# Performance work log

Measured on AMD Instinct MI355X. Metric: run time of the kernel, lower is better.

The kernel has to match this reference:

```python
import jax, jax.numpy as jnp
import numpy as np

B, S, D = 16, 4096, 1024
K = 65536  # number of keys == number of concepts (identity mapping)
EPS = 1e-12


def setup_inputs() -> dict:
    key = jax.random.key(0)
    k1, k2, k3, k4, k5, k6 = jax.random.split(key, 6)
    return {
        "hidden": jax.random.normal(k1, (B, S, D), dtype=jnp.float32),
        "concept_signal": jax.random.normal(k2, (B, 1, D), dtype=jnp.float32),
        "keys": jax.random.normal(k3, (K, D), dtype=jnp.float32),
        "values": jax.random.normal(k4, (K, 1, D), dtype=jnp.float32),
        "key_to_value": jnp.arange(K, dtype=jnp.int64),
        "W_layer": jax.random.normal(k5, (D, D), dtype=jnp.float32) * 0.02,
        "b_layer": jax.random.normal(k6, (D,), dtype=jnp.float32) * 0.02,
    }


def _l2norm(x, axis=-1):
    return x / jnp.maximum(jnp.linalg.norm(x, axis=axis, keepdims=True), EPS)


def reference(hidden, concept_signal, keys, values, key_to_value, W_layer, b_layer):
    # self.layer(hidden_state): Linear(D, D)
    layer_out = jnp.einsum("bsd,ed->bse", hidden, W_layer) + b_layer  # [B, S, D]

    # Tensor branch of forward: per-sample nearest-key search.
    # q: one query position per sample (P=1) -> [B, D]
    q = concept_signal[:, 0, :]
    cos = jnp.einsum("bd,kd->bk", _l2norm(q), _l2norm(keys))  # cosine similarity [B, K]
    dist = 1.0 - cos                                           # cosine distance
    chosen_key = jnp.argmin(dist, axis=1)                      # [B] nearest key per sample
    # s = 1 - smallest_dist; with threshold=-2.0 it always passes; with
    # max_tokens_per_concept=1, k = max(1, ceil(clamp(s,0,1)*1)) == 1 token.
    concept_idx = key_to_value[chosen_key]                     # [B]
    tokens = values[concept_idx, 0, :]                         # [B, D] (first of the k=1 tokens)
    tokens = _l2norm(tokens)                                   # F.normalize(..., p=2, dim=-1)
    # vstack one token onto each sample, then stack -> [B, S+1, D]
    return jnp.concatenate([layer_out, tokens[:, None, :]], axis=1)
```

## Files before the change

kernel.cpp:

```cpp
#include <hip/hip_runtime.h>

constexpr int BB = 16;
constexpr int SS = 4096;
constexpr int DD = 1024;
constexpr int KK = 65536;
constexpr int GM = BB * SS;
constexpr int GK = DD;

typedef __attribute__((ext_vector_type(8))) short bf16x8;
typedef __attribute__((ext_vector_type(4))) float f32x4;
typedef __attribute__((ext_vector_type(8))) unsigned short ushort8;

#define GLD_LDS16(g, l)                                                        \
  __builtin_amdgcn_global_load_lds(                                            \
      (const __attribute__((address_space(1))) void*)(g),                      \
      (__attribute__((address_space(3))) void*)(l), 16, 0, 0)

__device__ __forceinline__ unsigned short f2bf(float x) {
  unsigned u = __float_as_uint(x);
  u += 0x7fffu + ((u >> 16) & 1u);
  return (unsigned short)(u >> 16);
}

__global__ void cvt_bf16(const float* __restrict__ in,
                         unsigned short* __restrict__ out, int n8) {
  int stride = gridDim.x * blockDim.x;
  for (int i = blockIdx.x * blockDim.x + threadIdx.x; i < n8; i += stride) {
    const float4* p = (const float4*)in + (size_t)i * 2;
    float4 a = p[0], b = p[1];
    ushort8 r;
    r[0] = f2bf(a.x); r[1] = f2bf(a.y); r[2] = f2bf(a.z); r[3] = f2bf(a.w);
    r[4] = f2bf(b.x); r[5] = f2bf(b.y); r[6] = f2bf(b.z); r[7] = f2bf(b.w);
    *(ushort8*)(out + (size_t)i * 8) = r;
  }
}

__global__ __launch_bounds__(256) void qt_prep(const float* __restrict__ csig,
                                               float* __restrict__ qT) {
  int e = blockIdx.x * 256 + threadIdx.x;
  int b = e >> 10, d = e & 1023;
  qT[d * 16 + b] = csig[e];
}


#define LDA8(AH, BUF) do {                                                     \
  _Pragma("unroll") for (int ms = 0; ms < 4; ++ms) {                           \
    int rowa = (wm << 7) + ((AH) << 6) + (ms << 4) + fr;                       \
    _Pragma("unroll") for (int ks = 0; ks < 2; ++ks) {                         \
      int ia = ((rowa << 6) + (ks << 5) + (kg << 3)) ^ sw;                     \
      ar[ms * 2 + ks] = *(const bf16x8*)&lds[(BUF) + ia]; } }                  \
} while (0)

#define LDB4(NP, BUF) do {                                                     \
  _Pragma("unroll") for (int nn = 0; nn < 2; ++nn) {                           \
    int rowb = (wn << 6) + ((((NP) << 1) + nn) << 4) + fr;                     \
    _Pragma("unroll") for (int ks = 0; ks < 2; ++ks) {                         \
      int ib = ((rowb << 6) + (ks << 5) + (kg << 3)) ^ sw;                     \
      br[(((NP) << 1) + nn) * 2 + ks] = *(const bf16x8*)&lds[(BUF) + ib]; } }  \
} while (0)

#define MFMAQ(AH, NP) do {                                                     \
  _Pragma("unroll") for (int ms = 0; ms < 4; ++ms)                             \
  _Pragma("unroll") for (int nn = 0; nn < 2; ++nn)                             \
  _Pragma("unroll") for (int ks = 0; ks < 2; ++ks)                             \
    acc[((AH) << 2) + ms][((NP) << 1) + nn] =                                  \
      __builtin_amdgcn_mfma_f32_16x16x32_bf16(ar[ms * 2 + ks],                 \
        br[(((NP) << 1) + nn) * 2 + ks],                                       \
        acc[((AH) << 2) + ms][((NP) << 1) + nn], 0, 0, 0);                     \
} while (0)

#define STAGEQ(GB, LB, QJ)                                                     \
  GLD_LDS16((GB) + (size_t)(((QJ) << 6) + srq) * GK + ssc,                     \
            &lds[(LB) + ((((QJ) << 9) + (wv << 6)) << 3)])

#define PH_MID do { __builtin_amdgcn_s_barrier();                              \
  asm volatile("s_waitcnt lgkmcnt(0)" ::: "memory");                           \
  __builtin_amdgcn_sched_barrier(0);                                           \
  __builtin_amdgcn_s_setprio(1); } while (0)

#define PH_END do { __builtin_amdgcn_s_setprio(0);                             \
  __builtin_amdgcn_s_barrier(); } while (0)

#define PH_END_V(N) do { __builtin_amdgcn_s_setprio(0);                        \
  asm volatile("s_waitcnt vmcnt(" #N ")" ::: "memory");                        \
  __builtin_amdgcn_sched_barrier(0);                                           \
  __builtin_amdgcn_s_barrier(); } while (0)

__global__ __launch_bounds__(512, 2) void gemm8(
    const unsigned short* __restrict__ A,
    const unsigned short* __restrict__ Bm,
    const float* __restrict__ bias,
    float* __restrict__ out) {
  __shared__ unsigned short lds[65536];

  int g = blockIdx.x;
  int t = ((g & 7) << 7) + (g >> 3);
  int mt = t >> 2, nt = t & 3;
  int m0 = mt << 8, n0 = nt << 8;

  int tid = threadIdx.x, lane = tid & 63, wv = tid >> 6;
  int wm = wv >> 2, wn = wv & 3;
  int fr = lane & 15, kg = lane >> 4;
  int sw = (fr & 7) << 3;

  int srq = (wv << 3) + (lane >> 3);
  int ssc = (((lane & 7) ^ ((lane >> 3) & 7)) << 3);

  const unsigned short* Ag = A + (size_t)m0 * GK;
  const unsigned short* Bg = Bm + (size_t)n0 * GK;

  f32x4 acc[8][4] = {};
  bf16x8 ar[8], br[8];

  {
    const unsigned short* b0 = Bg;
    const unsigned short* a1 = Ag + 64;
    const unsigned short* b1 = Bg + 64;
    STAGEQ(Ag, 0, 0); STAGEQ(Ag, 0, 1); STAGEQ(Ag, 0, 2); STAGEQ(Ag, 0, 3);
    STAGEQ(b0, 16384, 0); STAGEQ(b0, 16384, 1);
    STAGEQ(b0, 16384, 2); STAGEQ(b0, 16384, 3);
    STAGEQ(a1, 32768, 0); STAGEQ(a1, 32768, 2);
    STAGEQ(b1, 49152, 0); STAGEQ(b1, 49152, 1);
    STAGEQ(b1, 49152, 2); STAGEQ(b1, 49152, 3);
    asm volatile("s_waitcnt vmcnt(6)" ::: "memory");
    __builtin_amdgcn_sched_barrier(0);
    __builtin_amdgcn_s_barrier();
  }

  for (int i = 0; i < 7; ++i) {
    const unsigned short* a1 = Ag + (size_t)(2 * i + 1) * 64;
    const unsigned short* a2 = Ag + (size_t)(2 * i + 2) * 64;
    const unsigned short* b2 = Bg + (size_t)(2 * i + 2) * 64;
    const unsigned short* a3 = Ag + (size_t)(2 * i + 3) * 64;
    const unsigned short* b3 = Bg + (size_t)(2 * i + 3) * 64;
    LDA8(0, 0); LDB4(0, 16384);
    STAGEQ(a1, 32768, 1); STAGEQ(a1, 32768, 3);
    PH_MID; MFMAQ(0, 0); PH_END;
    LDB4(1, 16384);
    STAGEQ(a2, 0, 0); STAGEQ(a2, 0, 2);
    PH_MID; MFMAQ(0, 1); PH_END;
    LDA8(1, 0);
    STAGEQ(b2, 16384, 0); STAGEQ(b2, 16384, 1);
    PH_MID; MFMAQ(1, 0); PH_END;
    STAGEQ(b2, 16384, 2); STAGEQ(b2, 16384, 3);
    PH_MID; MFMAQ(1, 1); PH_END_V(6);
    LDA8(0, 32768); LDB4(0, 49152);
    STAGEQ(a2, 0, 1); STAGEQ(a2, 0, 3);
    PH_MID; MFMAQ(0, 0); PH_END;
    LDB4(1, 49152);
    STAGEQ(a3, 32768, 0); STAGEQ(a3, 32768, 2);
    PH_MID; MFMAQ(0, 1); PH_END;
    LDA8(1, 32768);
    STAGEQ(b3, 49152, 0); STAGEQ(b3, 49152, 1);
    PH_MID; MFMAQ(1, 0); PH_END;
    STAGEQ(b3, 49152, 2); STAGEQ(b3, 49152, 3);
    PH_MID; MFMAQ(1, 1); PH_END_V(6);
  }

  {
    const unsigned short* a15 = Ag + (size_t)15 * 64;
    LDA8(0, 0); LDB4(0, 16384);
    STAGEQ(a15, 32768, 1); STAGEQ(a15, 32768, 3);
    PH_MID; MFMAQ(0, 0); PH_END;
    LDB4(1, 16384); PH_MID; MFMAQ(0, 1); PH_END;
    LDA8(1, 0);     PH_MID; MFMAQ(1, 0); PH_END;
    PH_MID; MFMAQ(1, 1); PH_END_V(0);
    LDA8(0, 32768); LDB4(0, 49152); PH_MID; MFMAQ(0, 0); PH_END;
    LDB4(1, 49152); PH_MID; MFMAQ(0, 1); PH_END;
    LDA8(1, 32768); PH_MID; MFMAQ(1, 0); PH_END;
    PH_MID; MFMAQ(1, 1);
    __builtin_amdgcn_s_setprio(0);
  }

  int r0 = kg << 2, cc = fr;
#pragma unroll
  for (int ni = 0; ni < 4; ++ni) {
    int gcol = n0 + (wn << 6) + (ni << 4) + cc;
    float bv = bias[gcol];
#pragma unroll
    for (int mi = 0; mi < 8; ++mi) {
      int gr = m0 + (wm << 7) + (mi << 4) + r0;
#pragma unroll
      for (int j = 0; j < 4; ++j) {
        int grow = gr + j;
        size_t o = ((size_t)(grow + (grow >> 12)) << 10) + gcol;
        out[o] = acc[mi][ni][j] + bv;
      }
    }
  }
}

__global__ __launch_bounds__(256) void cos_part4(
    const float* __restrict__ keys,
    const float* __restrict__ qT,
    float* __restrict__ pd,
    float* __restrict__ pn) {
  __shared__ float kt[32][256];
  __shared__ float qs[256 * 16];

  int tid = threadIdx.x;
  int kgrp = blockIdx.x & 255, dc = blockIdx.x >> 8;
  int k0 = kgrp << 8, d0 = dc << 8;

  {
    const float4* src = (const float4*)(qT + (size_t)d0 * 16);
    float4* dst = (float4*)qs;
#pragma unroll
    for (int i = 0; i < 4; ++i) dst[tid + i * 256] = src[tid + i * 256];
  }

  float acc[16] = {0.f, 0.f, 0.f, 0.f, 0.f, 0.f, 0.f, 0.f,
                   0.f, 0.f, 0.f, 0.f, 0.f, 0.f, 0.f, 0.f};
  float nrm = 0.f;

  int srow = tid >> 3, scol = (tid & 7) << 2;
  const float* gsrc = keys + (size_t)(k0 + srow) * DD + d0 + scol;

  float4 stg[8];
#pragma unroll
  for (int i = 0; i < 8; ++i)
    stg[i] = *(const float4*)(gsrc + (size_t)i * 32 * DD);

  for (int t = 0; t < 8; ++t) {
#pragma unroll
    for (int i = 0; i < 8; ++i) {
      int r = (i << 5) + srow;
#pragma unroll
      for (int j = 0; j < 4; ++j) {
        int dd = scol + j;
        kt[dd][r ^ (((dd >> 2) & 7) << 2)] = stg[i][j];
      }
    }
    __syncthreads();

    if (t + 1 < 8) {
#pragma unroll
      for (int i = 0; i < 8; ++i)
        stg[i] = *(const float4*)(gsrc + (size_t)i * 32 * DD + (t + 1) * 32);
    }

    const float* qb = qs + (t << 5) * 16;
#pragma unroll
    for (int dd = 0; dd < 32; ++dd) {
      float kv = kt[dd][tid ^ (((dd >> 2) & 7) << 2)];
      float4 q0 = *(const float4*)(qb + dd * 16 + 0);
      float4 q1 = *(const float4*)(qb + dd * 16 + 4);
      float4 q2 = *(const float4*)(qb + dd * 16 + 8);
      float4 q3 = *(const float4*)(qb + dd * 16 + 12);
      acc[0]  = fmaf(kv, q0.x, acc[0]);  acc[1]  = fmaf(kv, q0.y, acc[1]);
      acc[2]  = fmaf(kv, q0.z, acc[2]);  acc[3]  = fmaf(kv, q0.w, acc[3]);
      acc[4]  = fmaf(kv, q1.x, acc[4]);  acc[5]  = fmaf(kv, q1.y, acc[5]);
      acc[6]  = fmaf(kv, q1.z, acc[6]);  acc[7]  = fmaf(kv, q1.w, acc[7]);
      acc[8]  = fmaf(kv, q2.x, acc[8]);  acc[9]  = fmaf(kv, q2.y, acc[9]);
      acc[10] = fmaf(kv, q2.z, acc[10]); acc[11] = fmaf(kv, q2.w, acc[11]);
      acc[12] = fmaf(kv, q3.x, acc[12]); acc[13] = fmaf(kv, q3.y, acc[13]);
      acc[14] = fmaf(kv, q3.z, acc[14]); acc[15] = fmaf(kv, q3.w, acc[15]);
      nrm = fmaf(kv, kv, nrm);
    }
    __syncthreads();
  }

  int k = k0 + tid;
  float4* po = (float4*)(pd + ((size_t)dc * KK + k) * 16);
  po[0] = make_float4(acc[0], acc[1], acc[2], acc[3]);
  po[1] = make_float4(acc[4], acc[5], acc[6], acc[7]);
  po[2] = make_float4(acc[8], acc[9], acc[10], acc[11]);
  po[3] = make_float4(acc[12], acc[13], acc[14], acc[15]);
  pn[(size_t)dc * KK + k] = nrm;
}

__global__ __launch_bounds__(256) void cos_combine(
    const float* __restrict__ pd, const float* __restrict__ pn,
    float* __restrict__ pscore, int* __restrict__ pidx) {
  __shared__ float rs[4][16];
  __shared__ int ri[4][16];
  int tid = threadIdx.x, lane = tid & 63, w = tid >> 6;
  int k = blockIdx.x * 256 + tid;

  float d[16] = {0.f, 0.f, 0.f, 0.f, 0.f, 0.f, 0.f, 0.f,
                 0.f, 0.f, 0.f, 0.f, 0.f, 0.f, 0.f, 0.f};
  float nrm = 0.f;
#pragma unroll
  for (int dc = 0; dc < 4; ++dc) {
    const float4* p = (const float4*)(pd + ((size_t)dc * KK + k) * 16);
#pragma unroll
    for (int i = 0; i < 4; ++i) {
      float4 v = p[i];
      d[i * 4 + 0] += v.x; d[i * 4 + 1] += v.y;
      d[i * 4 + 2] += v.z; d[i * 4 + 3] += v.w;
    }
    nrm += pn[(size_t)dc * KK + k];
  }
  float inv = rsqrtf(fmaxf(nrm, 1e-24f));

#pragma unroll
  for (int b = 0; b < 16; ++b) {
    float s = d[b] * inv;
    int i = k;
#pragma unroll
    for (int off = 32; off; off >>= 1) {
      float s2 = __shfl_xor(s, off);
      int i2 = __shfl_xor(i, off);
      if (s2 > s || (s2 == s && i2 < i)) { s = s2; i = i2; }
    }
    if (lane == 0) { rs[w][b] = s; ri[w][b] = i; }
  }
  __syncthreads();
  if (tid < 16) {
    float bs = rs[0][tid]; int bi = ri[0][tid];
#pragma unroll
    for (int w2 = 1; w2 < 4; ++w2) {
      float s = rs[w2][tid]; int i = ri[w2][tid];
      if (s > bs || (s == bs && i < bi)) { bs = s; bi = i; }
    }
    pscore[(size_t)tid * gridDim.x + blockIdx.x] = bs;
    pidx[(size_t)tid * gridDim.x + blockIdx.x] = bi;
  }
}

__global__ __launch_bounds__(256) void select_write(
    const float* __restrict__ pscore, const int* __restrict__ pidx, int nb,
    const int* __restrict__ ktv, const float* __restrict__ values,
    float* __restrict__ out) {
  __shared__ float ss[4];
  __shared__ int si[4];
  __shared__ float snrm;
  __shared__ int swin;
  int b = blockIdx.x, tid = threadIdx.x, lane = tid & 63, wv = tid >> 6;

  float best = -1e30f;
  int bidx = 0x7fffffff;
  for (int t = tid; t < nb; t += 256) {
    float s = pscore[(size_t)b * nb + t];
    int i = pidx[(size_t)b * nb + t];
    if (s > best || (s == best && i < bidx)) { best = s; bidx = i; }
  }
#pragma unroll
  for (int off = 32; off; off >>= 1) {
    float s = __shfl_xor(best, off);
    int i = __shfl_xor(bidx, off);
    if (s > best || (s == best && i < bidx)) { best = s; bidx = i; }
  }
  if (lane == 0) { ss[wv] = best; si[wv] = bidx; }
  __syncthreads();
  if (tid == 0) {
    float bs = ss[0]; int bi = si[0];
    for (int w2 = 1; w2 < 4; ++w2)
      if (ss[w2] > bs || (ss[w2] == bs && si[w2] < bi)) { bs = ss[w2]; bi = si[w2]; }
    swin = ktv[bi];
  }
  __syncthreads();
  int idx = swin;

  float4 v = ((const float4*)(values + (size_t)idx * DD))[tid];
  float nrm = v.x * v.x + v.y * v.y + v.z * v.z + v.w * v.w;
#pragma unroll
  for (int off = 32; off; off >>= 1) nrm += __shfl_xor(nrm, off);
  if (lane == 0) ss[wv] = nrm;
  __syncthreads();
  if (tid == 0) snrm = rsqrtf(fmaxf(ss[0] + ss[1] + ss[2] + ss[3], 1e-24f));
  __syncthreads();
  float inv = snrm;

  float4 o;
  o.x = v.x * inv; o.y = v.y * inv; o.z = v.z * inv; o.w = v.w * inv;
  ((float4*)(out + (((size_t)b * (SS + 1) + SS) << 10)))[tid] = o;
}

extern "C" void kernel_launch(void* const* d_in, const int* in_sizes, int n_in,
                              void* d_out, int out_size, void* d_ws,
                              size_t ws_size, hipStream_t stream) {
  const float* hidden = (const float*)d_in[0];
  const float* csig   = (const float*)d_in[1];
  const float* keys   = (const float*)d_in[2];
  const float* values = (const float*)d_in[3];
  const int*   ktv    = (const int*)d_in[4];
  const float* W      = (const float*)d_in[5];
  const float* bias   = (const float*)d_in[6];
  float* out = (float*)d_out;

  char* ws = (char*)d_ws;
  size_t off = 0;
  unsigned short* hbf = (unsigned short*)(ws + off); off += (size_t)GM * GK * 2;
  unsigned short* wbf = (unsigned short*)(ws + off); off += (size_t)DD * GK * 2;
  float* pd     = (float*)(ws + off); off += (size_t)4 * KK * 16 * 4;
  float* pn     = (float*)(ws + off); off += (size_t)4 * KK * 4;
  float* pscore = (float*)(ws + off); off += (size_t)16 * 256 * 4;
  int*   pidx   = (int*)(ws + off);   off += (size_t)16 * 256 * 4;
  float* qT     = (float*)(ws + off); off += (size_t)DD * 16 * 4;

  cvt_bf16<<<4096, 256, 0, stream>>>(hidden, hbf, GM * GK / 8);
  cvt_bf16<<<512, 256, 0, stream>>>(W, wbf, DD * GK / 8);
  qt_prep<<<64, 256, 0, stream>>>(csig, qT);

  cos_part4<<<1024, 256, 0, stream>>>(keys, qT, pd, pn);
  cos_combine<<<256, 256, 0, stream>>>(pd, pn, pscore, pidx);

  gemm8<<<1024, 512, 0, stream>>>(hbf, wbf, bias, out);

  select_write<<<BB, 256, 0, stream>>>(pscore, pidx, 256, ktv, values, out);
}
```

Measured before the change: 396.5 us.

## Fuse fp32-to-bf16 conversion of hidden into GEMM A-tile staging

Drops the separate pass that converts the large hidden tensor to bf16. The GEMM now loads fp32 A tiles into registers, converts them in-kernel and writes bf16 to LDS, software-pipelined against the MFMA phases. This removes a full read and write of a 256 MB-scale intermediate and one launch. In exchange the GEMM reads twice the bytes for A, uses more VGPRs for the staging registers, and replaces async global-to-LDS loads with register round trips, which could hurt occupancy or overlap.

After: 573.4 us. +44.6%, slower.

```diff
diff --git a/kernel.cpp b/kernel.cpp
--- a/kernel.cpp
+++ b/kernel.cpp
@@ -73,12 +73,32 @@
   GLD_LDS16((GB) + (size_t)(((QJ) << 6) + srq) * GK + ssc,                     \
             &lds[(LB) + ((((QJ) << 9) + (wv << 6)) << 3)])
 
+#define ALD(R, TP, QA, QB) do {                                                \
+  const float* pa_ = (TP) + (size_t)(((QA) << 6) + srq) * GK + ssc;            \
+  const float* pb_ = (TP) + (size_t)(((QB) << 6) + srq) * GK + ssc;            \
+  R[0] = *(const float4*)pa_; R[1] = *(const float4*)(pa_ + 4);                \
+  R[2] = *(const float4*)pb_; R[3] = *(const float4*)(pb_ + 4);                \
+} while (0)
+
+#define AWR(LB, QA, QB, R) do {                                                \
+  ushort8 w0_, w1_;                                                            \
+  w0_[0] = f2bf(R[0].x); w0_[1] = f2bf(R[0].y); w0_[2] = f2bf(R[0].z);         \
+  w0_[3] = f2bf(R[0].w); w0_[4] = f2bf(R[1].x); w0_[5] = f2bf(R[1].y);         \
+  w0_[6] = f2bf(R[1].z); w0_[7] = f2bf(R[1].w);                                \
+  w1_[0] = f2bf(R[2].x); w1_[1] = f2bf(R[2].y); w1_[2] = f2bf(R[2].z);         \
+  w1_[3] = f2bf(R[2].w); w1_[4] = f2bf(R[3].x); w1_[5] = f2bf(R[3].y);         \
+  w1_[6] = f2bf(R[3].z); w1_[7] = f2bf(R[3].w);                                \
+  *(ushort8*)&lds[(LB) + ((((QA) << 9) + (wv << 6)) << 3) + (lane << 3)] = w0_;\
+  *(ushort8*)&lds[(LB) + ((((QB) << 9) + (wv << 6)) << 3) + (lane << 3)] = w1_;\
+} while (0)
+
 #define PH_MID do { __builtin_amdgcn_s_barrier();                              \
   asm volatile("s_waitcnt lgkmcnt(0)" ::: "memory");                           \
   __builtin_amdgcn_sched_barrier(0);                                           \
   __builtin_amdgcn_s_setprio(1); } while (0)
 
 #define PH_END do { __builtin_amdgcn_s_setprio(0);                             \
+  __builtin_amdgcn_sched_barrier(0);                                           \
   __builtin_amdgcn_s_barrier(); } while (0)
 
 #define PH_END_V(N) do { __builtin_amdgcn_s_setprio(0);                        \
@@ -87,7 +107,7 @@
   __builtin_amdgcn_s_barrier(); } while (0)
 
 __global__ __launch_bounds__(512, 2) void gemm8(
-    const unsigned short* __restrict__ A,
+    const float* __restrict__ A,
     const unsigned short* __restrict__ Bm,
     const float* __restrict__ bias,
     float* __restrict__ out) {
@@ -106,70 +126,64 @@
   int srq = (wv << 3) + (lane >> 3);
   int ssc = (((lane & 7) ^ ((lane >> 3) & 7)) << 3);
 
-  const unsigned short* Ag = A + (size_t)m0 * GK;
+  const float* Ag = A + (size_t)m0 * GK;
   const unsigned short* Bg = Bm + (size_t)n0 * GK;
 
   f32x4 acc[8][4] = {};
   bf16x8 ar[8], br[8];
+  float4 sAX[4], sAY[4];
 
   {
-    const unsigned short* b0 = Bg;
-    const unsigned short* a1 = Ag + 64;
-    const unsigned short* b1 = Bg + 64;
-    STAGEQ(Ag, 0, 0); STAGEQ(Ag, 0, 1); STAGEQ(Ag, 0, 2); STAGEQ(Ag, 0, 3);
-    STAGEQ(b0, 16384, 0); STAGEQ(b0, 16384, 1);
-    STAGEQ(b0, 16384, 2); STAGEQ(b0, 16384, 3);
-    STAGEQ(a1, 32768, 0); STAGEQ(a1, 32768, 2);
-    STAGEQ(b1, 49152, 0); STAGEQ(b1, 49152, 1);
-    STAGEQ(b1, 49152, 2); STAGEQ(b1, 49152, 3);
-    asm volatile("s_waitcnt vmcnt(6)" ::: "memory");
-    __builtin_amdgcn_sched_barrier(0);
-    __builtin_amdgcn_s_barrier();
-  }
-
-  for (int i = 0; i < 7; ++i) {
-    const unsigned short* a1 = Ag + (size_t)(2 * i + 1) * 64;
-    const unsigned short* a2 = Ag + (size_t)(2 * i + 2) * 64;
-    const unsigned short* b2 = Bg + (size_t)(2 * i + 2) * 64;
-    const unsigned short* a3 = Ag + (size_t)(2 * i + 3) * 64;
-    const unsigned short* b3 = Bg + (size_t)(2 * i + 3) * 64;
+    const float* a1 = Ag + 64;
+    const float* a2 = Ag + 128;
+    STAGEQ(Bg, 16384, 0); STAGEQ(Bg, 16384, 1);
+    STAGEQ(Bg, 16384, 2); STAGEQ(Bg, 16384, 3);
+    STAGEQ(Bg + 64, 49152, 0); STAGEQ(Bg + 64, 49152, 1);
+    STAGEQ(Bg + 64, 49152, 2); STAGEQ(Bg + 64, 49152, 3);
+    ALD(sAX, Ag, 0, 2); ALD(sAY, Ag, 1, 3);
+    AWR(0, 0, 2, sAX);  AWR(0, 1, 3, sAY);
+    ALD(sAX, a1, 0, 2);
+    AWR(32768, 0, 2, sAX);
+    ALD(sAX, a1, 1, 3);
+    ALD(sAY, a2, 0, 2);
+    __syncthreads();
+  }
+
+  for (int i = 0; i < 8; ++i) {
+    int e2 = 2 * i + 2 > 15 ? 15 : 2 * i + 2;
+    int o2 = 2 * i + 3 > 15 ? 15 : 2 * i + 3;
+    int e4 = 2 * i + 4 > 15 ? 15 : 2 * i + 4;
+    const float* aE2 = Ag + (size_t)e2 * 64;
+    const float* aO2 = Ag + (size_t)o2 * 64;
+    const float* aE4 = Ag + (size_t)e4 * 64;
+    const unsigned short* bE2 = Bg + (size_t)e2 * 64;
+    const unsigned short* bO2 = Bg + (size_t)o2 * 64;
     LDA8(0, 0); LDB4(0, 16384);
-    STAGEQ(a1, 32768, 1); STAGEQ(a1, 32768, 3);
+    AWR(32768, 1, 3, sAX);
     PH_MID; MFMAQ(0, 0); PH_END;
     LDB4(1, 16384);
-    STAGEQ(a2, 0, 0); STAGEQ(a2, 0, 2);
+    AWR(0, 0, 2, sAY);
     PH_MID; MFMAQ(0, 1); PH_END;
     LDA8(1, 0);
-    STAGEQ(b2, 16384, 0); STAGEQ(b2, 16384, 1);
+    ALD(sAX, aE2, 1, 3);
+    STAGEQ(bE2, 16384, 0); STAGEQ(bE2, 16384, 1);
     PH_MID; MFMAQ(1, 0); PH_END;
-    STAGEQ(b2, 16384, 2); STAGEQ(b2, 16384, 3);
-    PH_MID; MFMAQ(1, 1); PH_END_V(6);
+    ALD(sAY, aO2, 0, 2);
+    STAGEQ(bE2, 16384, 2); STAGEQ(bE2, 16384, 3);
+    PH_MID; MFMAQ(1, 1); PH_END_V(12);
     LDA8(0, 32768); LDB4(0, 49152);
-    STAGEQ(a2, 0, 1); STAGEQ(a2, 0, 3);
+    AWR(0, 1, 3, sAX);
     PH_MID; MFMAQ(0, 0); PH_END;
     LDB4(1, 49152);
-    STAGEQ(a3, 32768, 0); STAGEQ(a3, 32768, 2);
+    AWR(32768, 0, 2, sAY);
     PH_MID; MFMAQ(0, 1); PH_END;
     LDA8(1, 32768);
-    STAGEQ(b3, 49152, 0); STAGEQ(b3, 49152, 1);
+    ALD(sAX, aO2, 1, 3);
+    STAGEQ(bO2, 49152, 0); STAGEQ(bO2, 49152, 1);
     PH_MID; MFMAQ(1, 0); PH_END;
-    STAGEQ(b3, 49152, 2); STAGEQ(b3, 49152, 3);
-    PH_MID; MFMAQ(1, 1); PH_END_V(6);
-  }
-
-  {
-    const unsigned short* a15 = Ag + (size_t)15 * 64;
-    LDA8(0, 0); LDB4(0, 16384);
-    STAGEQ(a15, 32768, 1); STAGEQ(a15, 32768, 3);
-    PH_MID; MFMAQ(0, 0); PH_END;
-    LDB4(1, 16384); PH_MID; MFMAQ(0, 1); PH_END;
-    LDA8(1, 0);     PH_MID; MFMAQ(1, 0); PH_END;
-    PH_MID; MFMAQ(1, 1); PH_END_V(0);
-    LDA8(0, 32768); LDB4(0, 49152); PH_MID; MFMAQ(0, 0); PH_END;
-    LDB4(1, 49152); PH_MID; MFMAQ(0, 1); PH_END;
-    LDA8(1, 32768); PH_MID; MFMAQ(1, 0); PH_END;
-    PH_MID; MFMAQ(1, 1);
-    __builtin_amdgcn_s_setprio(0);
+    ALD(sAY, aE4, 0, 2);
+    STAGEQ(bO2, 49152, 2); STAGEQ(bO2, 49152, 3);
+    PH_MID; MFMAQ(1, 1); PH_END_V(12);
   }
 
   int r0 = kg << 2, cc = fr;
@@ -381,7 +395,6 @@
 
   char* ws = (char*)d_ws;
   size_t off = 0;
-  unsigned short* hbf = (unsigned short*)(ws + off); off += (size_t)GM * GK * 2;
   unsigned short* wbf = (unsigned short*)(ws + off); off += (size_t)DD * GK * 2;
   float* pd     = (float*)(ws + off); off += (size_t)4 * KK * 16 * 4;
   float* pn     = (float*)(ws + off); off += (size_t)4 * KK * 4;
@@ -389,14 +402,13 @@
   int*   pidx   = (int*)(ws + off);   off += (size_t)16 * 256 * 4;
   float* qT     = (float*)(ws + off); off += (size_t)DD * 16 * 4;
 
-  cvt_bf16<<<4096, 256, 0, stream>>>(hidden, hbf, GM * GK / 8);
   cvt_bf16<<<512, 256, 0, stream>>>(W, wbf, DD * GK / 8);
   qt_prep<<<64, 256, 0, stream>>>(csig, qT);
 
   cos_part4<<<1024, 256, 0, stream>>>(keys, qT, pd, pn);
   cos_combine<<<256, 256, 0, stream>>>(pd, pn, pscore, pidx);
 
-  gemm8<<<1024, 512, 0, stream>>>(hbf, wbf, bias, out);
+  gemm8<<<1024, 512, 0, stream>>>(hidden, wbf, bias, out);
 
   select_write<<<BB, 256, 0, stream>>>(pscore, pidx, 256, ktv, values, out);
 }
```

## Fuse cosine partials and bf16 conversions into one heterogeneous prep launch

Applied to the files above, without the earlier changes.

Merges the key-similarity partial kernel and the hidden and W bf16 conversions into a single launch. Block ranges pick which job a block runs, so the memory-bound conversion overlaps the similarity work and two launches go away. The query transpose kernel is removed, and the cosine loop now reads concept_signal straight from global memory with broadcast loads instead of staging it in LDS. A fallback path reuses workspace when it is too small. The risk is slower query reads and load imbalance between the two kinds of block.

After: 412.1 us. 3.9% more time.

```diff
diff --git a/kernel.cpp b/kernel.cpp
--- a/kernel.cpp
+++ b/kernel.cpp
@@ -22,24 +22,107 @@
   return (unsigned short)(u >> 16);
 }
 
+__device__ __forceinline__ void cvt_body(const float* __restrict__ in,
+                                         unsigned short* __restrict__ out,
+                                         int i) {
+  const float4* p = (const float4*)in + (size_t)i * 2;
+  float4 a = p[0], b = p[1];
+  ushort8 r;
+  r[0] = f2bf(a.x); r[1] = f2bf(a.y); r[2] = f2bf(a.z); r[3] = f2bf(a.w);
+  r[4] = f2bf(b.x); r[5] = f2bf(b.y); r[6] = f2bf(b.z); r[7] = f2bf(b.w);
+  *(ushort8*)(out + (size_t)i * 8) = r;
+}
+
+__device__ __forceinline__ void cos_body(const float* __restrict__ keys,
+                                         const float* __restrict__ csig,
+                                         float* __restrict__ pd,
+                                         float* __restrict__ pn,
+                                         float (*kt)[256], int bid, int tid) {
+  int kgrp = bid & 255, dc = bid >> 8;
+  int k0 = kgrp << 8, d0 = dc << 8;
+
+  float acc[16] = {0.f, 0.f, 0.f, 0.f, 0.f, 0.f, 0.f, 0.f,
+                   0.f, 0.f, 0.f, 0.f, 0.f, 0.f, 0.f, 0.f};
+  float nrm = 0.f;
+
+  int srow = tid >> 3, scol = (tid & 7) << 2;
+  const float* gsrc = keys + (size_t)(k0 + srow) * DD + d0 + scol;
+
+  float4 stg[8];
+#pragma unroll
+  for (int i = 0; i < 8; ++i)
+    stg[i] = *(const float4*)(gsrc + (size_t)i * 32 * DD);
+
+  for (int t = 0; t < 8; ++t) {
+#pragma unroll
+    for (int i = 0; i < 8; ++i) {
+      int r = (i << 5) + srow;
+#pragma unroll
+      for (int j = 0; j < 4; ++j) {
+        int dd = scol + j;
+        kt[dd][r ^ (((dd >> 2) & 7) << 2)] = stg[i][j];
+      }
+    }
+    __syncthreads();
+
+    if (t + 1 < 8) {
+#pragma unroll
+      for (int i = 0; i < 8; ++i)
+        stg[i] = *(const float4*)(gsrc + (size_t)i * 32 * DD + (t + 1) * 32);
+    }
+
+    const float* qb = csig + d0 + (t << 5);
+#pragma unroll
+    for (int dd = 0; dd < 32; ++dd) {
+      float kv = kt[dd][tid ^ (((dd >> 2) & 7) << 2)];
+#pragma unroll
+      for (int b = 0; b < 16; ++b)
+        acc[b] = fmaf(kv, qb[(size_t)b * DD + dd], acc[b]);
+      nrm = fmaf(kv, kv, nrm);
+    }
+    __syncthreads();
+  }
+
+  int k = k0 + tid;
+  float4* po = (float4*)(pd + ((size_t)dc * KK + k) * 16);
+  po[0] = make_float4(acc[0], acc[1], acc[2], acc[3]);
+  po[1] = make_float4(acc[4], acc[5], acc[6], acc[7]);
+  po[2] = make_float4(acc[8], acc[9], acc[10], acc[11]);
+  po[3] = make_float4(acc[12], acc[13], acc[14], acc[15]);
+  pn[(size_t)dc * KK + k] = nrm;
+}
+
+__global__ __launch_bounds__(256) void prep_fused(
+    const float* __restrict__ keys, const float* __restrict__ csig,
+    float* __restrict__ pd, float* __restrict__ pn,
+    const float* __restrict__ hidden, unsigned short* __restrict__ hbf,
+    const float* __restrict__ W, unsigned short* __restrict__ wbf) {
+  __shared__ float kt[32][256];
+  int bid = blockIdx.x, tid = threadIdx.x;
+  if (bid < 1024) {
+    cos_body(keys, csig, pd, pn, kt, bid, tid);
+  } else if (bid < 5120) {
+    int base = (bid - 1024) * 256 + tid;
+#pragma unroll
+    for (int r = 0; r < 8; ++r)
+      cvt_body(hidden, hbf, base + r * (4096 * 256));
+  } else {
+    cvt_body(W, wbf, (bid - 5120) * 256 + tid);
+  }
+}
+
+__global__ __launch_bounds__(256) void cos_part4_k(
+    const float* __restrict__ keys, const float* __restrict__ csig,
+    float* __restrict__ pd, float* __restrict__ pn) {
+  __shared__ float kt[32][256];
+  cos_body(keys, csig, pd, pn, kt, blockIdx.x, threadIdx.x);
+}
+
 __global__ void cvt_bf16(const float* __restrict__ in,
                          unsigned short* __restrict__ out, int n8) {
   int stride = gridDim.x * blockDim.x;
-  for (int i = blockIdx.x * blockDim.x + threadIdx.x; i < n8; i += stride) {
-    const float4* p = (const float4*)in + (size_t)i * 2;
-    float4 a = p[0], b = p[1];
-    ushort8 r;
-    r[0] = f2bf(a.x); r[1] = f2bf(a.y); r[2] = f2bf(a.z); r[3] = f2bf(a.w);
-    r[4] = f2bf(b.x); r[5] = f2bf(b.y); r[6] = f2bf(b.z); r[7] = f2bf(b.w);
-    *(ushort8*)(out + (size_t)i * 8) = r;
-  }
-}
-
-__global__ __launch_bounds__(256) void qt_prep(const float* __restrict__ csig,
-                                               float* __restrict__ qT) {
-  int e = blockIdx.x * 256 + threadIdx.x;
-  int b = e >> 10, d = e & 1023;
-  qT[d * 16 + b] = csig[e];
+  for (int i = blockIdx.x * blockDim.x + threadIdx.x; i < n8; i += stride)
+    cvt_body(in, out, i);
 }
 
 
@@ -190,85 +273,6 @@
   }
 }
 
-__global__ __launch_bounds__(256) void cos_part4(
-    const float* __restrict__ keys,
-    const float* __restrict__ qT,
-    float* __restrict__ pd,
-    float* __restrict__ pn) {
-  __shared__ float kt[32][256];
-  __shared__ float qs[256 * 16];
-
-  int tid = threadIdx.x;
-  int kgrp = blockIdx.x & 255, dc = blockIdx.x >> 8;
-  int k0 = kgrp << 8, d0 = dc << 8;
-
-  {
-    const float4* src = (const float4*)(qT + (size_t)d0 * 16);
-    float4* dst = (float4*)qs;
-#pragma unroll
-    for (int i = 0; i < 4; ++i) dst[tid + i * 256] = src[tid + i * 256];
-  }
-
-  float acc[16] = {0.f, 0.f, 0.f, 0.f, 0.f, 0.f, 0.f, 0.f,
-                   0.f, 0.f, 0.f, 0.f, 0.f, 0.f, 0.f, 0.f};
-  float nrm = 0.f;
-
-  int srow = tid >> 3, scol = (tid & 7) << 2;
-  const float* gsrc = keys + (size_t)(k0 + srow) * DD + d0 + scol;
-
-  float4 stg[8];
-#pragma unroll
-  for (int i = 0; i < 8; ++i)
-    stg[i] = *(const float4*)(gsrc + (size_t)i * 32 * DD);
-
-  for (int t = 0; t < 8; ++t) {
-#pragma unroll
-    for (int i = 0; i < 8; ++i) {
-      int r = (i << 5) + srow;
-#pragma unroll
-      for (int j = 0; j < 4; ++j) {
-        int dd = scol + j;
-        kt[dd][r ^ (((dd >> 2) & 7) << 2)] = stg[i][j];
-      }
-    }
-    __syncthreads();
-
-    if (t + 1 < 8) {
-#pragma unroll
-      for (int i = 0; i < 8; ++i)
-        stg[i] = *(const float4*)(gsrc + (size_t)i * 32 * DD + (t + 1) * 32);
-    }
-
-    const float* qb = qs + (t << 5) * 16;
-#pragma unroll
-    for (int dd = 0; dd < 32; ++dd) {
-      float kv = kt[dd][tid ^ (((dd >> 2) & 7) << 2)];
-      float4 q0 = *(const float4*)(qb + dd * 16 + 0);
-      float4 q1 = *(const float4*)(qb + dd * 16 + 4);
-      float4 q2 = *(const float4*)(qb + dd * 16 + 8);
-      float4 q3 = *(const float4*)(qb + dd * 16 + 12);
-      acc[0]  = fmaf(kv, q0.x, acc[0]);  acc[1]  = fmaf(kv, q0.y, acc[1]);
-      acc[2]  = fmaf(kv, q0.z, acc[2]);  acc[3]  = fmaf(kv, q0.w, acc[3]);
-      acc[4]  = fmaf(kv, q1.x, acc[4]);  acc[5]  = fmaf(kv, q1.y, acc[5]);
-      acc[6]  = fmaf(kv, q1.z, acc[6]);  acc[7]  = fmaf(kv, q1.w, acc[7]);
-      acc[8]  = fmaf(kv, q2.x, acc[8]);  acc[9]  = fmaf(kv, q2.y, acc[9]);
-      acc[10] = fmaf(kv, q2.z, acc[10]); acc[11] = fmaf(kv, q2.w, acc[11]);
-      acc[12] = fmaf(kv, q3.x, acc[12]); acc[13] = fmaf(kv, q3.y, acc[13]);
-      acc[14] = fmaf(kv, q3.z, acc[14]); acc[15] = fmaf(kv, q3.w, acc[15]);
-      nrm = fmaf(kv, kv, nrm);
-    }
-    __syncthreads();
-  }
-
-  int k = k0 + tid;
-  float4* po = (float4*)(pd + ((size_t)dc * KK + k) * 16);
-  po[0] = make_float4(acc[0], acc[1], acc[2], acc[3]);
-  po[1] = make_float4(acc[4], acc[5], acc[6], acc[7]);
-  po[2] = make_float4(acc[8], acc[9], acc[10], acc[11]);
-  po[3] = make_float4(acc[12], acc[13], acc[14], acc[15]);
-  pn[(size_t)dc * KK + k] = nrm;
-}
-
 __global__ __launch_bounds__(256) void cos_combine(
     const float* __restrict__ pd, const float* __restrict__ pn,
     float* __restrict__ pscore, int* __restrict__ pidx) {
@@ -380,23 +384,37 @@
   float* out = (float*)d_out;
 
   char* ws = (char*)d_ws;
-  size_t off = 0;
-  unsigned short* hbf = (unsigned short*)(ws + off); off += (size_t)GM * GK * 2;
-  unsigned short* wbf = (unsigned short*)(ws + off); off += (size_t)DD * GK * 2;
-  float* pd     = (float*)(ws + off); off += (size_t)4 * KK * 16 * 4;
-  float* pn     = (float*)(ws + off); off += (size_t)4 * KK * 4;
-  float* pscore = (float*)(ws + off); off += (size_t)16 * 256 * 4;
-  int*   pidx   = (int*)(ws + off);   off += (size_t)16 * 256 * 4;
-  float* qT     = (float*)(ws + off); off += (size_t)DD * 16 * 4;
-
-  cvt_bf16<<<4096, 256, 0, stream>>>(hidden, hbf, GM * GK / 8);
-  cvt_bf16<<<512, 256, 0, stream>>>(W, wbf, DD * GK / 8);
-  qt_prep<<<64, 256, 0, stream>>>(csig, qT);
-
-  cos_part4<<<1024, 256, 0, stream>>>(keys, qT, pd, pn);
-  cos_combine<<<256, 256, 0, stream>>>(pd, pn, pscore, pidx);
-
-  gemm8<<<1024, 512, 0, stream>>>(hbf, wbf, bias, out);
-
-  select_write<<<BB, 256, 0, stream>>>(pscore, pidx, 256, ktv, values, out);
-}
+  const size_t HB = (size_t)GM * GK * 2;
+  const size_t WB = (size_t)DD * GK * 2;
+  const size_t PDB = (size_t)4 * KK * 16 * 4;
+  const size_t PNB = (size_t)4 * KK * 4;
+  const size_t PSB = (size_t)16 * 256 * 4;
+
+  unsigned short* hbf = (unsigned short*)ws;
+  unsigned short* wbf = (unsigned short*)(ws + HB);
+
+  if (ws_size >= HB + WB + PDB + PNB + 2 * PSB) {
+    float* pd     = (float*)(ws + HB + WB);
+    float* pn     = (float*)(ws + HB + WB + PDB);
+    float* pscore = (float*)(ws + HB + WB + PDB + PNB);
+    int*   pidx   = (int*)(ws + HB + WB + PDB + PNB + PSB);
+
+    prep_fused<<<5632, 256, 0, stream>>>(keys, csig, pd, pn,
+                                         hidden, hbf, W, wbf);
+    cos_combine<<<256, 256, 0, stream>>>(pd, pn, pscore, pidx);
+    gemm8<<<1024, 512, 0, stream>>>(hbf, wbf, bias, out);
+    select_write<<<BB, 256, 0, stream>>>(pscore, pidx, 256, ktv, values, out);
+  } else {
+    float* pd     = (float*)ws;
+    float* pn     = (float*)(ws + PDB);
+    float* pscore = (float*)(ws + HB + WB);
+    int*   pidx   = (int*)(ws + HB + WB + PSB);
+
+    cos_part4_k<<<1024, 256, 0, stream>>>(keys, csig, pd, pn);
+    cos_combine<<<256, 256, 0, stream>>>(pd, pn, pscore, pidx);
+    cvt_bf16<<<4096, 256, 0, stream>>>(hidden, hbf, GM * GK / 8);
+    cvt_bf16<<<512, 256, 0, stream>>>(W, wbf, DD * GK / 8);
+    gemm8<<<1024, 512, 0, stream>>>(hbf, wbf, bias, out);
+    select_write<<<BB, 256, 0, stream>>>(pscore, pidx, 256, ktv, values, out);
+  }
+}
```

## Compute cosine search with split-bf16 MFMA and fused per-block argmax

Applied to the files above, without the earlier changes.

Replaces the FP32 FMA cosine-similarity kernel and its separate combine pass with a single MFMA kernel. The kernel splits queries and keys into bf16 high and low parts and uses three bf16 MFMAs to approximate fp32 accuracy. It also computes key norms and a per-block argmax inline, which removes the partial-dot workspace round trip and one kernel launch. The risk is a small precision loss from the three-term split, which could change argmin ties, and more select_write partials to reduce (1024 instead of 256).

Measured after the change: 379.9 us. 1.04x faster.

```diff
diff --git a/kernel.cpp b/kernel.cpp
--- a/kernel.cpp
+++ b/kernel.cpp
@@ -22,24 +22,112 @@
   return (unsigned short)(u >> 16);
 }
 
+__device__ __forceinline__ void cvt_body(const float* __restrict__ in,
+                                         unsigned short* __restrict__ out,
+                                         int i) {
+  const float4* p = (const float4*)in + (size_t)i * 2;
+  float4 a = p[0], b = p[1];
+  ushort8 r;
+  r[0] = f2bf(a.x); r[1] = f2bf(a.y); r[2] = f2bf(a.z); r[3] = f2bf(a.w);
+  r[4] = f2bf(b.x); r[5] = f2bf(b.y); r[6] = f2bf(b.z); r[7] = f2bf(b.w);
+  *(ushort8*)(out + (size_t)i * 8) = r;
+}
+
 __global__ void cvt_bf16(const float* __restrict__ in,
                          unsigned short* __restrict__ out, int n8) {
   int stride = gridDim.x * blockDim.x;
-  for (int i = blockIdx.x * blockDim.x + threadIdx.x; i < n8; i += stride) {
-    const float4* p = (const float4*)in + (size_t)i * 2;
-    float4 a = p[0], b = p[1];
-    ushort8 r;
-    r[0] = f2bf(a.x); r[1] = f2bf(a.y); r[2] = f2bf(a.z); r[3] = f2bf(a.w);
-    r[4] = f2bf(b.x); r[5] = f2bf(b.y); r[6] = f2bf(b.z); r[7] = f2bf(b.w);
-    *(ushort8*)(out + (size_t)i * 8) = r;
-  }
-}
-
-__global__ __launch_bounds__(256) void qt_prep(const float* __restrict__ csig,
-                                               float* __restrict__ qT) {
-  int e = blockIdx.x * 256 + threadIdx.x;
-  int b = e >> 10, d = e & 1023;
-  qT[d * 16 + b] = csig[e];
+  for (int i = blockIdx.x * blockDim.x + threadIdx.x; i < n8; i += stride)
+    cvt_body(in, out, i);
+}
+
+__global__ __launch_bounds__(256) void qsplit(const float* __restrict__ csig,
+                                              unsigned short* __restrict__ qh,
+                                              unsigned short* __restrict__ ql) {
+  int i = blockIdx.x * 256 + threadIdx.x;
+  float v = csig[i];
+  unsigned short h = f2bf(v);
+  float hf = __uint_as_float((unsigned)h << 16);
+  qh[i] = h;
+  ql[i] = f2bf(v - hf);
+}
+
+__global__ __launch_bounds__(256) void cos_mfma(
+    const float* __restrict__ keys,
+    const unsigned short* __restrict__ qh,
+    const unsigned short* __restrict__ ql,
+    float* __restrict__ pscore,
+    int* __restrict__ pidx) {
+  __shared__ float rs[4][16];
+  __shared__ int ri[4][16];
+  int tid = threadIdx.x, lane = tid & 63, w = tid >> 6;
+  int fr = lane & 15, kg = lane >> 4;
+  int key = blockIdx.x * 64 + w * 16 + fr;
+
+  const float* krow = keys + (size_t)key * DD + kg * 8;
+  const unsigned short* qhp = qh + fr * DD + kg * 8;
+  const unsigned short* qlp = ql + fr * DD + kg * 8;
+
+  f32x4 acc = {};
+  float nrm = 0.f;
+
+  float4 ka = *(const float4*)krow;
+  float4 kb = *(const float4*)(krow + 4);
+  bf16x8 h8 = *(const bf16x8*)qhp;
+  bf16x8 l8 = *(const bf16x8*)qlp;
+
+  for (int t = 0; t < 32; ++t) {
+    float4 kc = ka, kd = kb;
+    bf16x8 hh = h8, ll = l8;
+    if (t + 1 < 32) {
+      ka = *(const float4*)(krow + (t + 1) * 32);
+      kb = *(const float4*)(krow + (t + 1) * 32 + 4);
+      h8 = *(const bf16x8*)(qhp + (t + 1) * 32);
+      l8 = *(const bf16x8*)(qlp + (t + 1) * 32);
+    }
+    float ke[8] = {kc.x, kc.y, kc.z, kc.w, kd.x, kd.y, kd.z, kd.w};
+    ushort8 khv, klv;
+#pragma unroll
+    for (int j = 0; j < 8; ++j) {
+      float v = ke[j];
+      unsigned short h = f2bf(v);
+      float hf = __uint_as_float((unsigned)h << 16);
+      khv[j] = h;
+      klv[j] = f2bf(v - hf);
+      nrm = fmaf(v, v, nrm);
+    }
+    bf16x8 kh8 = *(bf16x8*)&khv, kl8 = *(bf16x8*)&klv;
+    acc = __builtin_amdgcn_mfma_f32_16x16x32_bf16(hh, kh8, acc, 0, 0, 0);
+    acc = __builtin_amdgcn_mfma_f32_16x16x32_bf16(ll, kh8, acc, 0, 0, 0);
+    acc = __builtin_amdgcn_mfma_f32_16x16x32_bf16(hh, kl8, acc, 0, 0, 0);
+  }
+
+  nrm += __shfl_xor(nrm, 16);
+  nrm += __shfl_xor(nrm, 32);
+  float inv = rsqrtf(fmaxf(nrm, 1e-24f));
+
+#pragma unroll
+  for (int j = 0; j < 4; ++j) {
+    float s = acc[j] * inv;
+    int i = key;
+#pragma unroll
+    for (int off = 1; off < 16; off <<= 1) {
+      float s2 = __shfl_xor(s, off);
+      int i2 = __shfl_xor(i, off);
+      if (s2 > s || (s2 == s && i2 < i)) { s = s2; i = i2; }
+    }
+    if (fr == 0) { rs[w][kg * 4 + j] = s; ri[w][kg * 4 + j] = i; }
+  }
+  __syncthreads();
+  if (tid < 16) {
+    float bs = rs[0][tid]; int bi = ri[0][tid];
+#pragma unroll
+    for (int w2 = 1; w2 < 4; ++w2) {
+      float s = rs[w2][tid]; int i = ri[w2][tid];
+      if (s > bs || (s == bs && i < bi)) { bs = s; bi = i; }
+    }
+    pscore[(size_t)tid * gridDim.x + blockIdx.x] = bs;
+    pidx[(size_t)tid * gridDim.x + blockIdx.x] = bi;
+  }
 }
 
 
@@ -190,134 +278,6 @@
   }
 }
 
-__global__ __launch_bounds__(256) void cos_part4(
-    const float* __restrict__ keys,
-    const float* __restrict__ qT,
-    float* __restrict__ pd,
-    float* __restrict__ pn) {
-  __shared__ float kt[32][256];
-  __shared__ float qs[256 * 16];
-
-  int tid = threadIdx.x;
-  int kgrp = blockIdx.x & 255, dc = blockIdx.x >> 8;
-  int k0 = kgrp << 8, d0 = dc << 8;
-
-  {
-    const float4* src = (const float4*)(qT + (size_t)d0 * 16);
-    float4* dst = (float4*)qs;
-#pragma unroll
-    for (int i = 0; i < 4; ++i) dst[tid + i * 256] = src[tid + i * 256];
-  }
-
-  float acc[16] = {0.f, 0.f, 0.f, 0.f, 0.f, 0.f, 0.f, 0.f,
-                   0.f, 0.f, 0.f, 0.f, 0.f, 0.f, 0.f, 0.f};
-  float nrm = 0.f;
-
-  int srow = tid >> 3, scol = (tid & 7) << 2;
-  const float* gsrc = keys + (size_t)(k0 + srow) * DD + d0 + scol;
-
-  float4 stg[8];
-#pragma unroll
-  for (int i = 0; i < 8; ++i)
-    stg[i] = *(const float4*)(gsrc + (size_t)i * 32 * DD);
-
-  for (int t = 0; t < 8; ++t) {
-#pragma unroll
-    for (int i = 0; i < 8; ++i) {
-      int r = (i << 5) + srow;
-#pragma unroll
-      for (int j = 0; j < 4; ++j) {
-        int dd = scol + j;
-        kt[dd][r ^ (((dd >> 2) & 7) << 2)] = stg[i][j];
-      }
-    }
-    __syncthreads();
-
-    if (t + 1 < 8) {
-#pragma unroll
-      for (int i = 0; i < 8; ++i)
-        stg[i] = *(const float4*)(gsrc + (size_t)i * 32 * DD + (t + 1) * 32);
-    }
-
-    const float* qb = qs + (t << 5) * 16;
-#pragma unroll
-    for (int dd = 0; dd < 32; ++dd) {
-      float kv = kt[dd][tid ^ (((dd >> 2) & 7) << 2)];
-      float4 q0 = *(const float4*)(qb + dd * 16 + 0);
-      float4 q1 = *(const float4*)(qb + dd * 16 + 4);
-      float4 q2 = *(const float4*)(qb + dd * 16 + 8);
-      float4 q3 = *(const float4*)(qb + dd * 16 + 12);
-      acc[0]  = fmaf(kv, q0.x, acc[0]);  acc[1]  = fmaf(kv, q0.y, acc[1]);
-      acc[2]  = fmaf(kv, q0.z, acc[2]);  acc[3]  = fmaf(kv, q0.w, acc[3]);
-      acc[4]  = fmaf(kv, q1.x, acc[4]);  acc[5]  = fmaf(kv, q1.y, acc[5]);
-      acc[6]  = fmaf(kv, q1.z, acc[6]);  acc[7]  = fmaf(kv, q1.w, acc[7]);
-      acc[8]  = fmaf(kv, q2.x, acc[8]);  acc[9]  = fmaf(kv, q2.y, acc[9]);
-      acc[10] = fmaf(kv, q2.z, acc[10]); acc[11] = fmaf(kv, q2.w, acc[11]);
-      acc[12] = fmaf(kv, q3.x, acc[12]); acc[13] = fmaf(kv, q3.y, acc[13]);
-      acc[14] = fmaf(kv, q3.z, acc[14]); acc[15] = fmaf(kv, q3.w, acc[15]);
-      nrm = fmaf(kv, kv, nrm);
-    }
-    __syncthreads();
-  }
-
-  int k = k0 + tid;
-  float4* po = (float4*)(pd + ((size_t)dc * KK + k) * 16);
-  po[0] = make_float4(acc[0], acc[1], acc[2], acc[3]);
-  po[1] = make_float4(acc[4], acc[5], acc[6], acc[7]);
-  po[2] = make_float4(acc[8], acc[9], acc[10], acc[11]);
-  po[3] = make_float4(acc[12], acc[13], acc[14], acc[15]);
-  pn[(size_t)dc * KK + k] = nrm;
-}
-
-__global__ __launch_bounds__(256) void cos_combine(
-    const float* __restrict__ pd, const float* __restrict__ pn,
-    float* __restrict__ pscore, int* __restrict__ pidx) {
-  __shared__ float rs[4][16];
-  __shared__ int ri[4][16];
-  int tid = threadIdx.x, lane = tid & 63, w = tid >> 6;
-  int k = blockIdx.x * 256 + tid;
-
-  float d[16] = {0.f, 0.f, 0.f, 0.f, 0.f, 0.f, 0.f, 0.f,
-                 0.f, 0.f, 0.f, 0.f, 0.f, 0.f, 0.f, 0.f};
-  float nrm = 0.f;
-#pragma unroll
-  for (int dc = 0; dc < 4; ++dc) {
-    const float4* p = (const float4*)(pd + ((size_t)dc * KK + k) * 16);
-#pragma unroll
-    for (int i = 0; i < 4; ++i) {
-      float4 v = p[i];
-      d[i * 4 + 0] += v.x; d[i * 4 + 1] += v.y;
-      d[i * 4 + 2] += v.z; d[i * 4 + 3] += v.w;
-    }
-    nrm += pn[(size_t)dc * KK + k];
-  }
-  float inv = rsqrtf(fmaxf(nrm, 1e-24f));
-
-#pragma unroll
-  for (int b = 0; b < 16; ++b) {
-    float s = d[b] * inv;
-    int i = k;
-#pragma unroll
-    for (int off = 32; off; off >>= 1) {
-      float s2 = __shfl_xor(s, off);
-      int i2 = __shfl_xor(i, off);
-      if (s2 > s || (s2 == s && i2 < i)) { s = s2; i = i2; }
-    }
-    if (lane == 0) { rs[w][b] = s; ri[w][b] = i; }
-  }
-  __syncthreads();
-  if (tid < 16) {
-    float bs = rs[0][tid]; int bi = ri[0][tid];
-#pragma unroll
-    for (int w2 = 1; w2 < 4; ++w2) {
-      float s = rs[w2][tid]; int i = ri[w2][tid];
-      if (s > bs || (s == bs && i < bi)) { bs = s; bi = i; }
-    }
-    pscore[(size_t)tid * gridDim.x + blockIdx.x] = bs;
-    pidx[(size_t)tid * gridDim.x + blockIdx.x] = bi;
-  }
-}
-
 __global__ __launch_bounds__(256) void select_write(
     const float* __restrict__ pscore, const int* __restrict__ pidx, int nb,
     const int* __restrict__ ktv, const float* __restrict__ values,
@@ -380,23 +340,26 @@
   float* out = (float*)d_out;
 
   char* ws = (char*)d_ws;
-  size_t off = 0;
-  unsigned short* hbf = (unsigned short*)(ws + off); off += (size_t)GM * GK * 2;
-  unsigned short* wbf = (unsigned short*)(ws + off); off += (size_t)DD * GK * 2;
-  float* pd     = (float*)(ws + off); off += (size_t)4 * KK * 16 * 4;
-  float* pn     = (float*)(ws + off); off += (size_t)4 * KK * 4;
-  float* pscore = (float*)(ws + off); off += (size_t)16 * 256 * 4;
-  int*   pidx   = (int*)(ws + off);   off += (size_t)16 * 256 * 4;
-  float* qT     = (float*)(ws + off); off += (size_t)DD * 16 * 4;
+  const size_t HB = (size_t)GM * GK * 2;
+  const size_t WB = (size_t)DD * GK * 2;
+  const size_t QB = (size_t)BB * DD * 2;
+  const size_t PSB = (size_t)BB * 1024 * 4;
+
+  unsigned short* hbf = (unsigned short*)ws;
+  unsigned short* wbf = (unsigned short*)(ws + HB);
+  unsigned short* qh  = (unsigned short*)(ws + HB + WB);
+  unsigned short* ql  = (unsigned short*)(ws + HB + WB + QB);
+  float* pscore = (float*)(ws + HB + WB + 2 * QB);
+  int*   pidx   = (int*)(ws + HB + WB + 2 * QB + PSB);
+
+  qsplit<<<64, 256, 0, stream>>>(csig, qh, ql);
+
+  cos_mfma<<<1024, 256, 0, stream>>>(keys, qh, ql, pscore, pidx);
 
   cvt_bf16<<<4096, 256, 0, stream>>>(hidden, hbf, GM * GK / 8);
   cvt_bf16<<<512, 256, 0, stream>>>(W, wbf, DD * GK / 8);
-  qt_prep<<<64, 256, 0, stream>>>(csig, qT);
-
-  cos_part4<<<1024, 256, 0, stream>>>(keys, qT, pd, pn);
-  cos_combine<<<256, 256, 0, stream>>>(pd, pn, pscore, pidx);
 
   gemm8<<<1024, 512, 0, stream>>>(hbf, wbf, bias, out);
 
-  select_write<<<BB, 256, 0, stream>>>(pscore, pidx, 256, ktv, values, out);
-}
+  select_write<<<BB, 256, 0, stream>>>(pscore, pidx, 1024, ktv, values, out);
+}
```
